# Performance work log

Measured on AMD Instinct MI355X. Metric: run time of the kernel, lower is better.

Reference implementation:

```python
import jax, jax.numpy as jnp
import numpy as np

N_NODES = 100000
N_EDGES = 1600000
F_IN, HIDDEN, N_CLASS = 256, 64, 2


def _gcn_conv(x, W, b, src, dst, norm, n):
    # PyG GCNConv: linear (no bias) -> normalized scatter-add -> bias
    h = x @ W                                  # [N, out]
    msg = h[src] * norm[:, None]               # gather + scale, [E+N, out]
    agg = jax.ops.segment_sum(msg, dst, num_segments=n)
    return agg + b


def setup_inputs() -> dict:
    key = jax.random.key(0)
    ks = jax.random.split(key, 8)
    x = jax.random.normal(ks[0], (N_NODES, F_IN), dtype=jnp.float32)
    edge_index = jax.random.randint(ks[1], (2, N_EDGES), 0, N_NODES, dtype=jnp.int32)
    W1 = jax.random.normal(ks[2], (F_IN, HIDDEN), dtype=jnp.float32) / np.sqrt(F_IN).astype(np.float32)
    b1 = jnp.zeros((HIDDEN,), dtype=jnp.float32)
    W2 = jax.random.normal(ks[3], (HIDDEN, HIDDEN), dtype=jnp.float32) / np.sqrt(HIDDEN).astype(np.float32)
    b2 = jnp.zeros((HIDDEN,), dtype=jnp.float32)
    W3 = jax.random.normal(ks[4], (HIDDEN, N_CLASS), dtype=jnp.float32) / np.sqrt(HIDDEN).astype(np.float32)
    b3 = jnp.zeros((N_CLASS,), dtype=jnp.float32)
    return {"x": x, "edge_index": edge_index, "W1": W1, "b1": b1, "W2": W2, "b2": b2, "W3": W3, "b3": b3}


def reference(x, edge_index, W1, b1, W2, b2, W3, b3):
    n = x.shape[0]
    # add self-loops (GCNConv default)
    loops = jnp.arange(n, dtype=edge_index.dtype)
    src = jnp.concatenate([edge_index[0], loops])
    dst = jnp.concatenate([edge_index[1], loops])
    # symmetric normalization D^-1/2 A_hat D^-1/2
    deg = jax.ops.segment_sum(jnp.ones_like(src, dtype=x.dtype), dst, num_segments=n)
    deg_inv_sqrt = jnp.where(deg > 0, jax.lax.rsqrt(jnp.maximum(deg, 1.0)), 0.0)
    norm = deg_inv_sqrt[src] * deg_inv_sqrt[dst]
    # layer 1 + relu (dropout is identity in eval mode)
    h = jax.nn.relu(_gcn_conv(x, W1, b1, src, dst, norm, n))
    # layer 2 + relu
    h = jax.nn.relu(_gcn_conv(h, W2, b2, src, dst, norm, n))
    # output layer + log_softmax
    h = _gcn_conv(h, W3, b3, src, dst, norm, n)
    return jax.nn.log_softmax(h, axis=1)
```

## Files before the change

kernel.cpp:

```cpp
#include <hip/hip_runtime.h>
#include <math.h>

#define F_IN 256
#define HID  64
#define BSH  8
#define BSPAN 256
#define CHUNK 4096
#define NBK_MAX 512

typedef __bf16   bf16x8 __attribute__((ext_vector_type(8)));
typedef float    floatx4 __attribute__((ext_vector_type(4)));
typedef _Float16 half8 __attribute__((ext_vector_type(8)));
typedef _Float16 half4v __attribute__((ext_vector_type(4)));

__global__ __launch_bounds__(256) void k_hist(const int* __restrict__ dst,
                                              int* __restrict__ cntT,
                                              int E, int NCH, int NBK) {
    __shared__ int hist[NBK_MAX];
    int t = threadIdx.x, c = blockIdx.x;
    hist[t] = 0; hist[t + 256] = 0;
    __syncthreads();
    int base = c * CHUNK;
#pragma unroll 4
    for (int j = 0; j < CHUNK / 256; j++) {
        int e = base + j * 256 + t;
        if (e < E) atomicAdd(&hist[dst[e] >> BSH], 1);
    }
    __syncthreads();
    for (int b = t; b < NBK; b += 256) cntT[b * NCH + c] = hist[b];
}

__global__ __launch_bounds__(256) void k_scanA(const int* __restrict__ cntT,
                                               int* __restrict__ off,
                                               int* __restrict__ partials, int S) {
    __shared__ int sh[256];
    int tid = threadIdx.x;
    int base = blockIdx.x * 1024 + tid * 4;
    int v[4];
    int s = 0;
#pragma unroll
    for (int j = 0; j < 4; j++) {
        int idx = base + j;
        v[j] = (idx < S) ? cntT[idx] : 0;
        s += v[j];
    }
    sh[tid] = s;
    __syncthreads();
    int mysum = s;
    for (int o = 1; o < 256; o <<= 1) {
        int tv = (tid >= o) ? sh[tid - o] : 0;
        __syncthreads();
        sh[tid] += tv;
        __syncthreads();
    }
    int pref = sh[tid] - mysum;
#pragma unroll
    for (int j = 0; j < 4; j++) {
        int idx = base + j;
        if (idx < S) off[idx] = pref;
        pref += v[j];
    }
    if (tid == 255) partials[blockIdx.x] = sh[255];
}

__global__ void k_scanB(int* __restrict__ partials, int* __restrict__ off,
                        int nblk, int S) {
    if (blockIdx.x == 0 && threadIdx.x == 0) {
        int run = 0;
        for (int b = 0; b < nblk; b++) { int t = partials[b]; partials[b] = run; run += t; }
        off[S] = run;
    }
}

__global__ void k_scanC(int* __restrict__ off, const int* __restrict__ partials, int S) {
    int i = blockIdx.x * blockDim.x + threadIdx.x;
    if (i < S) off[i] += partials[i >> 10];
}

__global__ __launch_bounds__(256) void k_sortwrite(const int* __restrict__ src,
                                                   const int* __restrict__ dst,
                                                   const int* __restrict__ off,
                                                   int* __restrict__ ebuf,
                                                   int E, int NCH, int NBK) {
    __shared__ int cur[NBK_MAX];
    int t = threadIdx.x, c = blockIdx.x;
    for (int b = t; b < NBK; b += 256) cur[b] = off[b * NCH + c];
    __syncthreads();
    int base = c * CHUNK;
#pragma unroll 4
    for (int j = 0; j < CHUNK / 256; j++) {
        int e = base + j * 256 + t;
        if (e < E) {
            int s = src[e];
            int d = dst[e];
            int pos = atomicAdd(&cur[d >> BSH], 1);
            ebuf[pos] = (s << BSH) | (d & (BSPAN - 1));
        }
    }
}

__global__ __launch_bounds__(256) void k_bucket_csr(const int* __restrict__ off,
                                                    const int* __restrict__ ebuf,
                                                    int* __restrict__ rp,
                                                    float* __restrict__ dinv,
                                                    int* __restrict__ esrc,
                                                    int N, int NCH, int NBK) {
    __shared__ int cnt[BSPAN];
    __shared__ int sh[BSPAN];
    int b = blockIdx.x, t = threadIdx.x;
    int base = off[b * NCH];
    int end  = off[(b + 1) * NCH];

    cnt[t] = 0;
    __syncthreads();
    for (int i = base + t; i < end; i += 256) atomicAdd(&cnt[ebuf[i] & (BSPAN - 1)], 1);
    __syncthreads();

    int c = cnt[t];
    sh[t] = c;
    __syncthreads();
    for (int o = 1; o < 256; o <<= 1) {
        int tv = (t >= o) ? sh[t - o] : 0;
        __syncthreads();
        sh[t] += tv;
        __syncthreads();
    }
    int excl = sh[t] - c;

    int node = (b << BSH) + t;
    if (node < N) {
        rp[node] = base + excl;
        dinv[node] = rsqrtf((float)(1 + c));
    }
    if (b == NBK - 1) {
        if (t == 0) rp[N] = end;
        if (t < 16) esrc[end + t] = 0;
    }
    __syncthreads();

    cnt[t] = base + excl;
    __syncthreads();
    for (int i = base + t; i < end; i += 256) {
        int v = ebuf[i];
        int p = atomicAdd(&cnt[v & (BSPAN - 1)], 1);
        esrc[p] = ((v >> BSH) << 6) | (v & 63);
    }
}

__global__ __launch_bounds__(256) void k_prepw(const float* __restrict__ W1,
                                               __bf16* __restrict__ f1h, __bf16* __restrict__ f1l,
                                               const float* __restrict__ W2,
                                               __bf16* __restrict__ f2h, __bf16* __restrict__ f2l) {
    int t = threadIdx.x + blockIdx.x * blockDim.x;
    for (int idx = t; idx < 16384; idx += 2048) {
        int j = idx & 7, lane = (idx >> 3) & 63, ch2 = (idx >> 9) & 7, c = idx >> 12;
        int k = ch2 * 32 + (lane >> 4) * 8 + j, col = c * 16 + (lane & 15);
        float w = W1[k * 64 + col];
        __bf16 h = (__bf16)w;
        f1h[idx] = h; f1l[idx] = (__bf16)(w - (float)h);
    }
    for (int idx = t; idx < 4096; idx += 2048) {
        int j = idx & 7, lane = (idx >> 3) & 63, ch2 = (idx >> 9) & 1, c = idx >> 10;
        int k = ch2 * 32 + (lane >> 4) * 8 + j, col = c * 16 + (lane & 15);
        float w = W2[k * 64 + col];
        __bf16 h = (__bf16)w;
        f2h[idx] = h; f2l[idx] = (__bf16)(w - (float)h);
    }
}

__global__ __launch_bounds__(256) void k_gemm1(const float* __restrict__ A,
                                               const __bf16* __restrict__ BfH,
                                               const __bf16* __restrict__ BfL,
                                               const float* __restrict__ dinv,
                                               _Float16* __restrict__ C, int nrows) {
    constexpr int K = 256, KC = 64, NCHK = 4, NCH32 = 8;
    __shared__ float As[2][64 * KC];

    const int t = threadIdx.x;
    const int wave = t >> 6, lane = t & 63;
    const int m = lane & 15, q = lane >> 4;
    const int row0 = blockIdx.x * 64;

    const int s_sub = lane >> 4;
    const int s_seg = lane & 15;

    auto stage = [&](int ch, int buf) {
#pragma unroll
        for (int j = 0; j < 4; j++) {
            int lr = wave * 16 + j * 4 + s_sub;
            int gr = row0 + lr; if (gr > nrows - 1) gr = nrows - 1;
            int gs = (s_seg - lr) & 15;
            const float* g = A + (size_t)gr * K + ch * KC + gs * 4;
            float* l = &As[buf][(size_t)lr * KC + s_seg * 4];
            __builtin_amdgcn_global_load_lds(
                (const __attribute__((address_space(1))) void*)g,
                (__attribute__((address_space(3))) void*)l, 16, 0, 0);
        }
    };

    floatx4 acc[4] = {{0.f, 0.f, 0.f, 0.f}, {0.f, 0.f, 0.f, 0.f},
                      {0.f, 0.f, 0.f, 0.f}, {0.f, 0.f, 0.f, 0.f}};

    stage(0, 0);
    __syncthreads();

    for (int ch = 0; ch < NCHK; ch++) {
        if (ch + 1 < NCHK) stage(ch + 1, (ch + 1) & 1);

        const float* arow = &As[ch & 1][(size_t)(wave * 16 + m) * KC];
#pragma unroll
        for (int jj = 0; jj < 2; jj++) {
            int ch2 = ch * 2 + jj;
            int s0 = jj * 8 + q * 2;
            float4 v0 = *(const float4*)(arow + (((s0 + m) & 15) * 4));
            float4 v1 = *(const float4*)(arow + (((s0 + 1 + m) & 15) * 4));
            float af[8] = {v0.x, v0.y, v0.z, v0.w, v1.x, v1.y, v1.z, v1.w};
            bf16x8 ah, al;
#pragma unroll
            for (int j = 0; j < 8; j++) {
                __bf16 h = (__bf16)af[j];
                ah[j] = h;
                al[j] = (__bf16)(af[j] - (float)h);
            }
#pragma unroll
            for (int c = 0; c < 4; c++) {
                const bf16x8 bh = *(const bf16x8*)(BfH + ((size_t)(c * NCH32 + ch2) * 64 + lane) * 8);
                const bf16x8 bl = *(const bf16x8*)(BfL + ((size_t)(c * NCH32 + ch2) * 64 + lane) * 8);
                acc[c] = __builtin_amdgcn_mfma_f32_16x16x32_bf16(ah, bh, acc[c], 0, 0, 0);
                acc[c] = __builtin_amdgcn_mfma_f32_16x16x32_bf16(al, bh, acc[c], 0, 0, 0);
                acc[c] = __builtin_amdgcn_mfma_f32_16x16x32_bf16(ah, bl, acc[c], 0, 0, 0);
            }
        }
        __syncthreads();
    }

#pragma unroll
    for (int i = 0; i < 4; i++) {
        int r = row0 + wave * 16 + q * 4 + i;
        if (r < nrows) {
            float di = dinv[r];
#pragma unroll
            for (int c = 0; c < 4; c++)
                C[(size_t)r * 64 + c * 16 + m] = (_Float16)(acc[c][i] * di);
        }
    }
}

__global__ __launch_bounds__(256) void k_gemm2(const _Float16* __restrict__ A,
                                               const __bf16* __restrict__ BfH,
                                               const __bf16* __restrict__ BfL,
                                               const float* __restrict__ dinv,
                                               _Float16* __restrict__ C, int nrows) {
    __shared__ _Float16 As[64 * 64];
    const int t = threadIdx.x;
    const int wave = t >> 6, lane = t & 63;
    const int m = lane & 15, q = lane >> 4;
    const int row0 = blockIdx.x * 64;

#pragma unroll
    for (int j = 0; j < 2; j++) {
        int lr = j * 32 + wave * 8 + (lane >> 3);
        int p  = lane & 7;
        int gr = row0 + lr; if (gr > nrows - 1) gr = nrows - 1;
        int gs = (p - lr) & 7;
        const _Float16* g = A + (size_t)gr * 64 + gs * 8;
        _Float16* l = &As[(size_t)lr * 64 + p * 8];
        __builtin_amdgcn_global_load_lds(
            (const __attribute__((address_space(1))) void*)g,
            (__attribute__((address_space(3))) void*)l, 16, 0, 0);
    }
    __syncthreads();

    floatx4 acc[4] = {{0.f, 0.f, 0.f, 0.f}, {0.f, 0.f, 0.f, 0.f},
                      {0.f, 0.f, 0.f, 0.f}, {0.f, 0.f, 0.f, 0.f}};

    const _Float16* arow = &As[(size_t)(wave * 16 + m) * 64];
#pragma unroll
    for (int jj = 0; jj < 2; jj++) {
        int s0 = jj * 4 + q;
        half8 v = *(const half8*)(arow + (((s0 + m) & 7) * 8));
        bf16x8 ah, al;
#pragma unroll
        for (int j = 0; j < 8; j++) {
            float f = (float)v[j];
            __bf16 h = (__bf16)f;
            ah[j] = h;
            al[j] = (__bf16)(f - (float)h);
        }
#pragma unroll
        for (int c = 0; c < 4; c++) {
            const bf16x8 bh = *(const bf16x8*)(BfH + ((size_t)(c * 2 + jj) * 64 + lane) * 8);
            const bf16x8 bl = *(const bf16x8*)(BfL + ((size_t)(c * 2 + jj) * 64 + lane) * 8);
            acc[c] = __builtin_amdgcn_mfma_f32_16x16x32_bf16(ah, bh, acc[c], 0, 0, 0);
            acc[c] = __builtin_amdgcn_mfma_f32_16x16x32_bf16(al, bh, acc[c], 0, 0, 0);
            acc[c] = __builtin_amdgcn_mfma_f32_16x16x32_bf16(ah, bl, acc[c], 0, 0, 0);
        }
    }

#pragma unroll
    for (int i = 0; i < 4; i++) {
        int r = row0 + wave * 16 + q * 4 + i;
        if (r < nrows) {
            float di = dinv[r];
#pragma unroll
            for (int c = 0; c < 4; c++)
                C[(size_t)r * 64 + c * 16 + m] = (_Float16)(acc[c][i] * di);
        }
    }
}

template <int MODE>
__global__ __launch_bounds__(256) void k_aggE(const _Float16* __restrict__ hs,
                                              const float* __restrict__ dinv,
                                              const int* __restrict__ rp,
                                              const int* __restrict__ esrc,
                                              const float* __restrict__ bias,
                                              const float* __restrict__ W3,
                                              void* __restrict__ out, int n) {
    constexpr int NPB = 64;
    constexpr int LDW = 68;
    __shared__ float acc[NPB * LDW];

    const int t = threadIdx.x;
    const int wv = t >> 6, lane = t & 63;
    const int qe = lane >> 4, fg = lane & 15;
    const int nb = blockIdx.x * NPB;
    const int ne = min(nb + NPB, n);

    for (int i = t; i < NPB * LDW; i += 256) acc[i] = 0.f;

    const int eb0 = rp[nb];
    const int eb1 = rp[ne];
    __syncthreads();

    const int L  = eb1 - eb0;
    const int wl = (L + 3) >> 2;
    const int wa = eb0 + wv * wl;
    const int wb = min(wa + wl, eb1);
    const int ql = (wl + 3) >> 2;
    const int qa = wa + qe * ql;
    const int qb = min(qa + ql, wb);

    int cur = -1;
    floatx4 r = {0.f, 0.f, 0.f, 0.f};
    for (int e = qa; e < qb; e += 8) {
        int ev[8]; half4v v[8];
#pragma unroll
        for (int u = 0; u < 8; u++) {
            ev[u] = esrc[e + u];
            v[u]  = *(const half4v*)(hs + (size_t)(ev[u] >> 6) * 64 + fg * 4);
        }
#pragma unroll
        for (int u = 0; u < 8; u++) {
            if (e + u < qb) {
                int row = ev[u] & 63;
                float f0 = (float)v[u][0], f1 = (float)v[u][1];
                float f2 = (float)v[u][2], f3 = (float)v[u][3];
                if (row != cur) {
                    if (cur >= 0) {
                        float* a = &acc[cur * LDW + fg * 4];
                        atomicAdd(a + 0, r[0]); atomicAdd(a + 1, r[1]);
                        atomicAdd(a + 2, r[2]); atomicAdd(a + 3, r[3]);
                    }
                    cur = row;
                    r[0] = f0; r[1] = f1; r[2] = f2; r[3] = f3;
                } else {
                    r[0] += f0; r[1] += f1; r[2] += f2; r[3] += f3;
                }
            }
        }
    }
    if (cur >= 0) {
        float* a = &acc[cur * LDW + fg * 4];
        atomicAdd(a + 0, r[0]); atomicAdd(a + 1, r[1]);
        atomicAdd(a + 2, r[2]); atomicAdd(a + 3, r[3]);
    }
    __syncthreads();

    if (MODE == 0) {
#pragma unroll
        for (int it = 0; it < 4; it++) {
            int nl = it * 16 + (t >> 4);
            int node = nb + nl;
            if (node < n) {
                int f = (t & 15) * 4;
                float dii = dinv[node];
                floatx4 av = *(const floatx4*)&acc[nl * LDW + f];
                half4v sv = *(const half4v*)(hs + (size_t)node * 64 + f);
                float4 b4 = ((const float4*)bias)[t & 15];
                float v0 = fmaxf((av[0] + (float)sv[0]) * dii + b4.x, 0.f);
                float v1 = fmaxf((av[1] + (float)sv[1]) * dii + b4.y, 0.f);
                float v2 = fmaxf((av[2] + (float)sv[2]) * dii + b4.z, 0.f);
                float v3 = fmaxf((av[3] + (float)sv[3]) * dii + b4.w, 0.f);
                half4v o4;
                o4[0] = (_Float16)v0; o4[1] = (_Float16)v1;
                o4[2] = (_Float16)v2; o4[3] = (_Float16)v3;
                *(half4v*)((_Float16*)out + (size_t)node * 64 + f) = o4;
            }
        }
    } else {
        for (int it = 0; it < 16; it++) {
            int nl = it * 4 + wv;
            int node = nb + nl;
            if (node >= n) break;
            float dii = dinv[node];
            float a = acc[nl * LDW + lane] + (float)hs[(size_t)node * 64 + lane];
            a = fmaxf(a * dii + bias[lane], 0.f);
            float2 w = ((const float2*)W3)[lane];
            float p0 = a * w.x, p1 = a * w.y;
#pragma unroll
            for (int o = 1; o <= 32; o <<= 1) {
                p0 += __shfl_xor(p0, o, 64);
                p1 += __shfl_xor(p1, o, 64);
            }
            if (lane == 0) ((float2*)out)[node] = make_float2(p0 * dii, p1 * dii);
        }
    }
}

__global__ __launch_bounds__(256) void k_final(const float2* __restrict__ h3s,
                                               const float* __restrict__ dinv,
                                               const int* __restrict__ rp,
                                               const int* __restrict__ esrc,
                                               const float* __restrict__ b3,
                                               float* __restrict__ out, int n) {
    int i = blockIdx.x * blockDim.x + threadIdx.x;
    if (i >= n) return;
    float dii = dinv[i];
    float2 h = h3s[i];
    float ax = h.x, ay = h.y;
    float bx = 0.f, by = 0.f, cx = 0.f, cy = 0.f, dx = 0.f, dy = 0.f;
    int e0 = rp[i], e1 = rp[i + 1];
    for (int e = e0; e < e1; e += 4) {
        int last = e1 - 1;
        int s0 = esrc[e] >> 6;
        int s1 = esrc[min(e + 1, last)] >> 6;
        int s2 = esrc[min(e + 2, last)] >> 6;
        int s3 = esrc[min(e + 3, last)] >> 6;
        float2 v0 = h3s[s0];
        float2 v1 = h3s[s1];
        float2 v2 = h3s[s2];
        float2 v3 = h3s[s3];
        ax += v0.x; ay += v0.y;
        bx += (e + 1 <= last) ? v1.x : 0.f; by += (e + 1 <= last) ? v1.y : 0.f;
        cx += (e + 2 <= last) ? v2.x : 0.f; cy += (e + 2 <= last) ? v2.y : 0.f;
        dx += (e + 3 <= last) ? v3.x : 0.f; dy += (e + 3 <= last) ? v3.y : 0.f;
    }
    float l0 = ((ax + bx) + (cx + dx)) * dii + b3[0];
    float l1 = ((ay + by) + (cy + dy)) * dii + b3[1];
    float mx = fmaxf(l0, l1);
    float lse = mx + log1pf(__expf(-fabsf(l0 - l1)));
    ((float2*)out)[i] = make_float2(l0 - lse, l1 - lse);
}

extern "C" void kernel_launch(void* const* d_in, const int* in_sizes, int n_in,
                              void* d_out, int out_size, void* d_ws, size_t ws_size,
                              hipStream_t stream) {
    const float* x   = (const float*)d_in[0];
    const int*   ei  = (const int*)d_in[1];
    const float* W1  = (const float*)d_in[2];
    const float* b1  = (const float*)d_in[3];
    const float* W2  = (const float*)d_in[4];
    const float* b2  = (const float*)d_in[5];
    const float* W3  = (const float*)d_in[6];
    const float* b3  = (const float*)d_in[7];
    float* out = (float*)d_out;

    const int N = in_sizes[0] / F_IN;
    const int E = in_sizes[1] / 2;
    const int* src = ei;
    const int* dst = ei + E;

    const int NBK = (N + BSPAN - 1) / BSPAN;
    const int NCH = (E + CHUNK - 1) / CHUNK;
    const int S   = NBK * NCH;

    char* p = (char*)d_ws;
    auto alloc = [&](size_t bytes) -> void* {
        void* r = (void*)p;
        p += (bytes + 255) & ~(size_t)255;
        return r;
    };
    int*      cntT     = (int*)alloc((size_t)S * 4);
    int*      off      = (int*)alloc((size_t)(S + 1) * 4);
    int*      partials = (int*)alloc(4096);
    int*      ebuf     = (int*)alloc((size_t)E * 4);
    int*      esrc     = (int*)alloc((size_t)(E + 64) * 4);
    int*      rp       = (int*)alloc((size_t)(N + 1) * 4);
    float*    dinv     = (float*)alloc((size_t)N * 4);
    _Float16* bufA     = (_Float16*)alloc((size_t)N * HID * 2);
    _Float16* bufB     = (_Float16*)alloc((size_t)N * HID * 2);
    float*    h3       = (float*)alloc((size_t)N * 2 * 4);
    __bf16*   f1h      = (__bf16*)alloc(16384 * 2);
    __bf16*   f1l      = (__bf16*)alloc(16384 * 2);
    __bf16*   f2h      = (__bf16*)alloc(4096 * 2);
    __bf16*   f2l      = (__bf16*)alloc(4096 * 2);

    const int T = 256;
    int scanBlocks = (S + 1023) / 1024;

    k_prepw<<<8, T, 0, stream>>>(W1, f1h, f1l, W2, f2h, f2l);

    k_hist<<<NCH, T, 0, stream>>>(dst, cntT, E, NCH, NBK);
    k_scanA<<<scanBlocks, T, 0, stream>>>(cntT, off, partials, S);
    k_scanB<<<1, 64, 0, stream>>>(partials, off, scanBlocks, S);
    k_scanC<<<(S + T - 1) / T, T, 0, stream>>>(off, partials, S);
    k_sortwrite<<<NCH, T, 0, stream>>>(src, dst, off, ebuf, E, NCH, NBK);
    k_bucket_csr<<<NBK, T, 0, stream>>>(off, ebuf, rp, dinv, esrc, N, NCH, NBK);

    int gemmBlocks = (N + 63) / 64;
    int aggBlocks  = (N + 63) / 64;
    k_gemm1<<<gemmBlocks, T, 0, stream>>>(x, f1h, f1l, dinv, bufA, N);
    k_aggE<0><<<aggBlocks, T, 0, stream>>>(bufA, dinv, rp, esrc, b1, nullptr, bufB, N);

    k_gemm2<<<gemmBlocks, T, 0, stream>>>(bufB, f2h, f2l, dinv, bufA, N);
    k_aggE<1><<<aggBlocks, T, 0, stream>>>(bufA, dinv, rp, esrc, b2, W3, h3, N);

    k_final<<<(N + T - 1) / T, T, 0, stream>>>((const float2*)h3, dinv, rp, esrc, b3, out, N);
}
```

Before: 406.6 us.

## Restructure edge aggregation: 32-node blocks, 8-wide half loads, double-buffered gathers

The aggregation kernel now handles 32 nodes per block instead of 64. Each lane covers 8 features with half8 loads, and the block's edge range is split into 32 segments, one per group of 8 lanes. Gathers are double-buffered in groups of four, so the next loads are in flight while the current group is accumulated. The packed edge encoding now stores the local row in 5 bits instead of 6 to match the smaller block, with matching shifts in the CSR build and final kernel. The aim is wider memory transactions and more memory-level parallelism, at the cost of more blocks and more flushes into shared-memory atomics.

```diff
diff --git a/kernel.cpp b/kernel.cpp
--- a/kernel.cpp
+++ b/kernel.cpp
@@ -143,7 +143,7 @@
     for (int i = base + t; i < end; i += 256) {
         int v = ebuf[i];
         int p = atomicAdd(&cnt[v & (BSPAN - 1)], 1);
-        esrc[p] = ((v >> BSH) << 6) | (v & 63);
+        esrc[p] = ((v >> BSH) << 5) | (v & 31);
     }
 }
 
@@ -309,6 +309,25 @@
     }
 }
 
+#define LOADB(EVa, EVb, EVc, EVd, Va, Vb, Vc, Vd, E) do {                     \
+    int _x0 = min((E),     sbm1);                                             \
+    int _x1 = min((E) + 1, sbm1);                                             \
+    int _x2 = min((E) + 2, sbm1);                                             \
+    int _x3 = min((E) + 3, sbm1);                                             \
+    EVa = esrc[_x0]; EVb = esrc[_x1]; EVc = esrc[_x2]; EVd = esrc[_x3];       \
+    Va = *(const half8*)(hs + (size_t)(EVa >> 5) * 64 + f8 * 8);              \
+    Vb = *(const half8*)(hs + (size_t)(EVb >> 5) * 64 + f8 * 8);              \
+    Vc = *(const half8*)(hs + (size_t)(EVc >> 5) * 64 + f8 * 8);              \
+    Vd = *(const half8*)(hs + (size_t)(EVd >> 5) * 64 + f8 * 8);              \
+} while (0)
+
+#define ACCB(EVa, EVb, EVc, EVd, Va, Vb, Vc, Vd, E) do {                      \
+    if ((E)     < sb) step(EVa, Va);                                          \
+    if ((E) + 1 < sb) step(EVb, Vb);                                          \
+    if ((E) + 2 < sb) step(EVc, Vc);                                          \
+    if ((E) + 3 < sb) step(EVd, Vd);                                          \
+} while (0)
+
 template <int MODE>
 __global__ __launch_bounds__(256) void k_aggE(const _Float16* __restrict__ hs,
                                               const float* __restrict__ dinv,
@@ -317,13 +336,14 @@
                                               const float* __restrict__ bias,
                                               const float* __restrict__ W3,
                                               void* __restrict__ out, int n) {
-    constexpr int NPB = 64;
+    constexpr int NPB = 32;
     constexpr int LDW = 68;
     __shared__ float acc[NPB * LDW];
 
     const int t = threadIdx.x;
     const int wv = t >> 6, lane = t & 63;
-    const int qe = lane >> 4, fg = lane & 15;
+    const int qe = lane >> 3;
+    const int f8 = lane & 7;
     const int nb = blockIdx.x * NPB;
     const int ne = min(nb + NPB, n);
 
@@ -333,87 +353,95 @@
     const int eb1 = rp[ne];
     __syncthreads();
 
-    const int L  = eb1 - eb0;
-    const int wl = (L + 3) >> 2;
-    const int wa = eb0 + wv * wl;
-    const int wb = min(wa + wl, eb1);
-    const int ql = (wl + 3) >> 2;
-    const int qa = wa + qe * ql;
-    const int qb = min(qa + ql, wb);
+    const int L   = eb1 - eb0;
+    const int sl  = (L + 31) >> 5;
+    const int sid = wv * 8 + qe;
+    const int sa  = eb0 + sid * sl;
+    const int sb  = min(sa + sl, eb1);
 
     int cur = -1;
-    floatx4 r = {0.f, 0.f, 0.f, 0.f};
-    for (int e = qa; e < qb; e += 8) {
-        int ev[8]; half4v v[8];
-#pragma unroll
-        for (int u = 0; u < 8; u++) {
-            ev[u] = esrc[e + u];
-            v[u]  = *(const half4v*)(hs + (size_t)(ev[u] >> 6) * 64 + fg * 4);
-        }
-#pragma unroll
-        for (int u = 0; u < 8; u++) {
-            if (e + u < qb) {
-                int row = ev[u] & 63;
-                float f0 = (float)v[u][0], f1 = (float)v[u][1];
-                float f2 = (float)v[u][2], f3 = (float)v[u][3];
-                if (row != cur) {
-                    if (cur >= 0) {
-                        float* a = &acc[cur * LDW + fg * 4];
-                        atomicAdd(a + 0, r[0]); atomicAdd(a + 1, r[1]);
-                        atomicAdd(a + 2, r[2]); atomicAdd(a + 3, r[3]);
-                    }
-                    cur = row;
-                    r[0] = f0; r[1] = f1; r[2] = f2; r[3] = f3;
-                } else {
-                    r[0] += f0; r[1] += f1; r[2] += f2; r[3] += f3;
-                }
+    float a0 = 0.f, a1 = 0.f, a2 = 0.f, a3 = 0.f;
+    float a4 = 0.f, a5 = 0.f, a6 = 0.f, a7 = 0.f;
+
+    auto flush = [&]() {
+        float* ap = &acc[cur * LDW + f8 * 8];
+        atomicAdd(ap + 0, a0); atomicAdd(ap + 1, a1);
+        atomicAdd(ap + 2, a2); atomicAdd(ap + 3, a3);
+        atomicAdd(ap + 4, a4); atomicAdd(ap + 5, a5);
+        atomicAdd(ap + 6, a6); atomicAdd(ap + 7, a7);
+    };
+    auto step = [&](int ev, half8 v) {
+        int row = ev & 31;
+        float f0 = (float)v[0], f1 = (float)v[1], f2 = (float)v[2], f3 = (float)v[3];
+        float f4 = (float)v[4], f5 = (float)v[5], f6 = (float)v[6], f7 = (float)v[7];
+        if (row != cur) {
+            if (cur >= 0) flush();
+            cur = row;
+            a0 = f0; a1 = f1; a2 = f2; a3 = f3;
+            a4 = f4; a5 = f5; a6 = f6; a7 = f7;
+        } else {
+            a0 += f0; a1 += f1; a2 += f2; a3 += f3;
+            a4 += f4; a5 += f5; a6 += f6; a7 += f7;
+        }
+    };
+
+    if (sa < sb) {
+        const int sbm1 = sb - 1;
+        int eA0, eA1, eA2, eA3; half8 vA0, vA1, vA2, vA3;
+        int eB0, eB1, eB2, eB3; half8 vB0, vB1, vB2, vB3;
+        int e = sa;
+        LOADB(eA0, eA1, eA2, eA3, vA0, vA1, vA2, vA3, e);
+        for (; e + 8 < sb; e += 8) {
+            LOADB(eB0, eB1, eB2, eB3, vB0, vB1, vB2, vB3, e + 4);
+            ACCB(eA0, eA1, eA2, eA3, vA0, vA1, vA2, vA3, e);
+            LOADB(eA0, eA1, eA2, eA3, vA0, vA1, vA2, vA3, e + 8);
+            ACCB(eB0, eB1, eB2, eB3, vB0, vB1, vB2, vB3, e + 4);
+        }
+        ACCB(eA0, eA1, eA2, eA3, vA0, vA1, vA2, vA3, e);
+        if (e + 4 < sb) {
+            LOADB(eB0, eB1, eB2, eB3, vB0, vB1, vB2, vB3, e + 4);
+            ACCB(eB0, eB1, eB2, eB3, vB0, vB1, vB2, vB3, e + 4);
+        }
+        if (cur >= 0) flush();
+    }
+    __syncthreads();
+
+    if (MODE == 0) {
+        int nl = t >> 3, f = (t & 7) * 8;
+        int node = nb + nl;
+        if (node < n) {
+            float dii = dinv[node];
+            const float* ap = &acc[nl * LDW + f];
+            half8 sv = *(const half8*)(hs + (size_t)node * 64 + f);
+            float4 b0 = ((const float4*)bias)[(t & 7) * 2];
+            float4 b1 = ((const float4*)bias)[(t & 7) * 2 + 1];
+            float bb[8] = {b0.x, b0.y, b0.z, b0.w, b1.x, b1.y, b1.z, b1.w};
+            half8 o;
+#pragma unroll
+            for (int j = 0; j < 8; j++) {
+                float val = (ap[j] + (float)sv[j]) * dii + bb[j];
+                o[j] = (_Float16)fmaxf(val, 0.f);
             }
-        }
-    }
-    if (cur >= 0) {
-        float* a = &acc[cur * LDW + fg * 4];
-        atomicAdd(a + 0, r[0]); atomicAdd(a + 1, r[1]);
-        atomicAdd(a + 2, r[2]); atomicAdd(a + 3, r[3]);
-    }
-    __syncthreads();
-
-    if (MODE == 0) {
-#pragma unroll
-        for (int it = 0; it < 4; it++) {
-            int nl = it * 16 + (t >> 4);
+            *(half8*)((_Float16*)out + (size_t)node * 64 + f) = o;
+        }
+    } else {
+#pragma unroll
+        for (int it = 0; it < 8; it++) {
+            int nl = it * 4 + wv;
             int node = nb + nl;
             if (node < n) {
-                int f = (t & 15) * 4;
                 float dii = dinv[node];
-                floatx4 av = *(const floatx4*)&acc[nl * LDW + f];
-                half4v sv = *(const half4v*)(hs + (size_t)node * 64 + f);
-                float4 b4 = ((const float4*)bias)[t & 15];
-                float v0 = fmaxf((av[0] + (float)sv[0]) * dii + b4.x, 0.f);
-                float v1 = fmaxf((av[1] + (float)sv[1]) * dii + b4.y, 0.f);
-                float v2 = fmaxf((av[2] + (float)sv[2]) * dii + b4.z, 0.f);
-                float v3 = fmaxf((av[3] + (float)sv[3]) * dii + b4.w, 0.f);
-                half4v o4;
-                o4[0] = (_Float16)v0; o4[1] = (_Float16)v1;
-                o4[2] = (_Float16)v2; o4[3] = (_Float16)v3;
-                *(half4v*)((_Float16*)out + (size_t)node * 64 + f) = o4;
+                float a = acc[nl * LDW + lane] + (float)hs[(size_t)node * 64 + lane];
+                a = fmaxf(a * dii + bias[lane], 0.f);
+                float2 w = ((const float2*)W3)[lane];
+                float p0 = a * w.x, p1 = a * w.y;
+#pragma unroll
+                for (int o = 1; o <= 32; o <<= 1) {
+                    p0 += __shfl_xor(p0, o, 64);
+                    p1 += __shfl_xor(p1, o, 64);
+                }
+                if (lane == 0) ((float2*)out)[node] = make_float2(p0 * dii, p1 * dii);
             }
-        }
-    } else {
-        for (int it = 0; it < 16; it++) {
-            int nl = it * 4 + wv;
-            int node = nb + nl;
-            if (node >= n) break;
-            float dii = dinv[node];
-            float a = acc[nl * LDW + lane] + (float)hs[(size_t)node * 64 + lane];
-            a = fmaxf(a * dii + bias[lane], 0.f);
-            float2 w = ((const float2*)W3)[lane];
-            float p0 = a * w.x, p1 = a * w.y;
-#pragma unroll
-            for (int o = 1; o <= 32; o <<= 1) {
-                p0 += __shfl_xor(p0, o, 64);
-                p1 += __shfl_xor(p1, o, 64);
-            }
-            if (lane == 0) ((float2*)out)[node] = make_float2(p0 * dii, p1 * dii);
         }
     }
 }
@@ -433,10 +461,10 @@
     int e0 = rp[i], e1 = rp[i + 1];
     for (int e = e0; e < e1; e += 4) {
         int last = e1 - 1;
-        int s0 = esrc[e] >> 6;
-        int s1 = esrc[min(e + 1, last)] >> 6;
-        int s2 = esrc[min(e + 2, last)] >> 6;
-        int s3 = esrc[min(e + 3, last)] >> 6;
+        int s0 = esrc[e] >> 5;
+        int s1 = esrc[min(e + 1, last)] >> 5;
+        int s2 = esrc[min(e + 2, last)] >> 5;
+        int s3 = esrc[min(e + 3, last)] >> 5;
         float2 v0 = h3s[s0];
         float2 v1 = h3s[s1];
         float2 v2 = h3s[s2];
@@ -509,7 +537,7 @@
     k_bucket_csr<<<NBK, T, 0, stream>>>(off, ebuf, rp, dinv, esrc, N, NCH, NBK);
 
     int gemmBlocks = (N + 63) / 64;
-    int aggBlocks  = (N + 63) / 64;
+    int aggBlocks  = (N + 31) / 32;
     k_gemm1<<<gemmBlocks, T, 0, stream>>>(x, f1h, f1l, dinv, bufA, N);
     k_aggE<0><<<aggBlocks, T, 0, stream>>>(bufA, dinv, rp, esrc, b1, nullptr, bufB, N);
 
```

Result: slower. 439.0 us (+8.0%).

## Store hidden features as four 16-column planes and restructure edge aggregation per plane

Applied to the files above, without the earlier changes.

The GEMM outputs and aggregation inputs move from row-major [N,64] fp16 to four planar [N,16] slices. Each plane is 32 bytes per node, so a pair of lanes covers one node per plane. The aggregation kernel now gives each lane pair a contiguous edge segment (128 segments per block) and loops over the four planes. Each lane gathers 16-byte half8 vectors, keeping the gathered working set per pass smaller and more cache-friendly. The cost is re-reading the edge indices four times, and the longer per-lane segments risk load imbalance and more LDS atomic flushes.

```diff
diff --git a/kernel.cpp b/kernel.cpp
--- a/kernel.cpp
+++ b/kernel.cpp
@@ -11,7 +11,6 @@
 typedef __bf16   bf16x8 __attribute__((ext_vector_type(8)));
 typedef float    floatx4 __attribute__((ext_vector_type(4)));
 typedef _Float16 half8 __attribute__((ext_vector_type(8)));
-typedef _Float16 half4v __attribute__((ext_vector_type(4)));
 
 __global__ __launch_bounds__(256) void k_hist(const int* __restrict__ dst,
                                               int* __restrict__ cntT,
@@ -180,6 +179,7 @@
     const int wave = t >> 6, lane = t & 63;
     const int m = lane & 15, q = lane >> 4;
     const int row0 = blockIdx.x * 64;
+    const size_t N16 = (size_t)nrows * 16;
 
     const int s_sub = lane >> 4;
     const int s_seg = lane & 15;
@@ -241,7 +241,7 @@
             float di = dinv[r];
 #pragma unroll
             for (int c = 0; c < 4; c++)
-                C[(size_t)r * 64 + c * 16 + m] = (_Float16)(acc[c][i] * di);
+                C[(size_t)c * N16 + (size_t)r * 16 + m] = (_Float16)(acc[c][i] * di);
         }
     }
 }
@@ -256,6 +256,7 @@
     const int wave = t >> 6, lane = t & 63;
     const int m = lane & 15, q = lane >> 4;
     const int row0 = blockIdx.x * 64;
+    const size_t N16 = (size_t)nrows * 16;
 
 #pragma unroll
     for (int j = 0; j < 2; j++) {
@@ -263,7 +264,7 @@
         int p  = lane & 7;
         int gr = row0 + lr; if (gr > nrows - 1) gr = nrows - 1;
         int gs = (p - lr) & 7;
-        const _Float16* g = A + (size_t)gr * 64 + gs * 8;
+        const _Float16* g = A + (size_t)(gs >> 1) * N16 + (size_t)gr * 16 + (gs & 1) * 8;
         _Float16* l = &As[(size_t)lr * 64 + p * 8];
         __builtin_amdgcn_global_load_lds(
             (const __attribute__((address_space(1))) void*)g,
@@ -304,10 +305,37 @@
             float di = dinv[r];
 #pragma unroll
             for (int c = 0; c < 4; c++)
-                C[(size_t)r * 64 + c * 16 + m] = (_Float16)(acc[c][i] * di);
-        }
-    }
-}
+                C[(size_t)c * N16 + (size_t)r * 16 + m] = (_Float16)(acc[c][i] * di);
+        }
+    }
+}
+
+#define FLUSH() do {                                                          \
+    float* ap = accph + cur * LDW;                                            \
+    atomicAdd(ap + 0, a0); atomicAdd(ap + 1, a1);                             \
+    atomicAdd(ap + 2, a2); atomicAdd(ap + 3, a3);                             \
+    atomicAdd(ap + 4, a4); atomicAdd(ap + 5, a5);                             \
+    atomicAdd(ap + 6, a6); atomicAdd(ap + 7, a7);                             \
+} while (0)
+
+#define STEPE(W, V, COND) do {                                                \
+    if (COND) {                                                               \
+        int row = (W) & 63;                                                   \
+        float f0 = (float)(V)[0], f1 = (float)(V)[1];                         \
+        float f2 = (float)(V)[2], f3 = (float)(V)[3];                         \
+        float f4 = (float)(V)[4], f5 = (float)(V)[5];                         \
+        float f6 = (float)(V)[6], f7 = (float)(V)[7];                         \
+        if (row != cur) {                                                     \
+            if (cur >= 0) FLUSH();                                            \
+            cur = row;                                                        \
+            a0 = f0; a1 = f1; a2 = f2; a3 = f3;                               \
+            a4 = f4; a5 = f5; a6 = f6; a7 = f7;                               \
+        } else {                                                              \
+            a0 += f0; a1 += f1; a2 += f2; a3 += f3;                           \
+            a4 += f4; a5 += f5; a6 += f6; a7 += f7;                           \
+        }                                                                     \
+    }                                                                         \
+} while (0)
 
 template <int MODE>
 __global__ __launch_bounds__(256) void k_aggE(const _Float16* __restrict__ hs,
@@ -323,9 +351,11 @@
 
     const int t = threadIdx.x;
     const int wv = t >> 6, lane = t & 63;
-    const int qe = lane >> 4, fg = lane & 15;
+    const int qe = lane >> 1;
+    const int f8 = lane & 1;
     const int nb = blockIdx.x * NPB;
     const int ne = min(nb + NPB, n);
+    const size_t N16 = (size_t)n * 16;
 
     for (int i = t; i < NPB * LDW; i += 256) acc[i] = 0.f;
 
@@ -333,87 +363,81 @@
     const int eb1 = rp[ne];
     __syncthreads();
 
-    const int L  = eb1 - eb0;
-    const int wl = (L + 3) >> 2;
-    const int wa = eb0 + wv * wl;
-    const int wb = min(wa + wl, eb1);
-    const int ql = (wl + 3) >> 2;
-    const int qa = wa + qe * ql;
-    const int qb = min(qa + ql, wb);
-
-    int cur = -1;
-    floatx4 r = {0.f, 0.f, 0.f, 0.f};
-    for (int e = qa; e < qb; e += 8) {
-        int ev[8]; half4v v[8];
-#pragma unroll
-        for (int u = 0; u < 8; u++) {
-            ev[u] = esrc[e + u];
-            v[u]  = *(const half4v*)(hs + (size_t)(ev[u] >> 6) * 64 + fg * 4);
-        }
-#pragma unroll
-        for (int u = 0; u < 8; u++) {
-            if (e + u < qb) {
-                int row = ev[u] & 63;
-                float f0 = (float)v[u][0], f1 = (float)v[u][1];
-                float f2 = (float)v[u][2], f3 = (float)v[u][3];
-                if (row != cur) {
-                    if (cur >= 0) {
-                        float* a = &acc[cur * LDW + fg * 4];
-                        atomicAdd(a + 0, r[0]); atomicAdd(a + 1, r[1]);
-                        atomicAdd(a + 2, r[2]); atomicAdd(a + 3, r[3]);
-                    }
-                    cur = row;
-                    r[0] = f0; r[1] = f1; r[2] = f2; r[3] = f3;
-                } else {
-                    r[0] += f0; r[1] += f1; r[2] += f2; r[3] += f3;
-                }
+    const int L   = eb1 - eb0;
+    const int sl  = (L + 127) >> 7;
+    const int sid = wv * 32 + qe;
+    const int sa  = eb0 + sid * sl;
+    const int sb  = min(sa + sl, eb1);
+
+    if (sa < sb) {
+        const int sbm1 = sb - 1;
+        for (int ph = 0; ph < 4; ph++) {
+            const _Float16* __restrict__ plane = hs + (size_t)ph * N16 + f8 * 8;
+            float* __restrict__ accph = acc + ph * 16 + f8 * 8;
+            int cur = -1;
+            float a0 = 0.f, a1 = 0.f, a2 = 0.f, a3 = 0.f;
+            float a4 = 0.f, a5 = 0.f, a6 = 0.f, a7 = 0.f;
+            for (int e = sa; e < sb; e += 4) {
+                int x1 = min(e + 1, sbm1);
+                int x2 = min(e + 2, sbm1);
+                int x3 = min(e + 3, sbm1);
+                int w0 = esrc[e], w1 = esrc[x1], w2 = esrc[x2], w3 = esrc[x3];
+                half8 v0 = *(const half8*)(plane + (size_t)(unsigned)(w0 >> 6) * 16);
+                half8 v1 = *(const half8*)(plane + (size_t)(unsigned)(w1 >> 6) * 16);
+                half8 v2 = *(const half8*)(plane + (size_t)(unsigned)(w2 >> 6) * 16);
+                half8 v3 = *(const half8*)(plane + (size_t)(unsigned)(w3 >> 6) * 16);
+                STEPE(w0, v0, true);
+                STEPE(w1, v1, e + 1 < sb);
+                STEPE(w2, v2, e + 2 < sb);
+                STEPE(w3, v3, e + 3 < sb);
             }
-        }
-    }
-    if (cur >= 0) {
-        float* a = &acc[cur * LDW + fg * 4];
-        atomicAdd(a + 0, r[0]); atomicAdd(a + 1, r[1]);
-        atomicAdd(a + 2, r[2]); atomicAdd(a + 3, r[3]);
+            FLUSH();
+        }
     }
     __syncthreads();
 
     if (MODE == 0) {
-#pragma unroll
-        for (int it = 0; it < 4; it++) {
-            int nl = it * 16 + (t >> 4);
-            int node = nb + nl;
-            if (node < n) {
-                int f = (t & 15) * 4;
-                float dii = dinv[node];
-                floatx4 av = *(const floatx4*)&acc[nl * LDW + f];
-                half4v sv = *(const half4v*)(hs + (size_t)node * 64 + f);
-                float4 b4 = ((const float4*)bias)[t & 15];
-                float v0 = fmaxf((av[0] + (float)sv[0]) * dii + b4.x, 0.f);
-                float v1 = fmaxf((av[1] + (float)sv[1]) * dii + b4.y, 0.f);
-                float v2 = fmaxf((av[2] + (float)sv[2]) * dii + b4.z, 0.f);
-                float v3 = fmaxf((av[3] + (float)sv[3]) * dii + b4.w, 0.f);
-                half4v o4;
-                o4[0] = (_Float16)v0; o4[1] = (_Float16)v1;
-                o4[2] = (_Float16)v2; o4[3] = (_Float16)v3;
-                *(half4v*)((_Float16*)out + (size_t)node * 64 + f) = o4;
+        int nl = t >> 2, ph = t & 3;
+        int node = nb + nl;
+        if (node < n) {
+            float dii = dinv[node];
+            const float* ap = &acc[nl * LDW + ph * 16];
+            const _Float16* sp = hs + (size_t)ph * N16 + (size_t)node * 16;
+            _Float16* op = (_Float16*)out + (size_t)ph * N16 + (size_t)node * 16;
+            const float4* bp = (const float4*)(bias + ph * 16);
+            float4 b0 = bp[0], b1 = bp[1], b2 = bp[2], b3 = bp[3];
+            float bb[16] = {b0.x, b0.y, b0.z, b0.w, b1.x, b1.y, b1.z, b1.w,
+                            b2.x, b2.y, b2.z, b2.w, b3.x, b3.y, b3.z, b3.w};
+            half8 s0 = *(const half8*)sp;
+            half8 s1 = *(const half8*)(sp + 8);
+            half8 o0, o1;
+#pragma unroll
+            for (int j = 0; j < 8; j++) {
+                o0[j] = (_Float16)fmaxf((ap[j] + (float)s0[j]) * dii + bb[j], 0.f);
+                o1[j] = (_Float16)fmaxf((ap[8 + j] + (float)s1[j]) * dii + bb[8 + j], 0.f);
             }
+            *(half8*)op = o0;
+            *(half8*)(op + 8) = o1;
         }
     } else {
+#pragma unroll
         for (int it = 0; it < 16; it++) {
             int nl = it * 4 + wv;
             int node = nb + nl;
-            if (node >= n) break;
-            float dii = dinv[node];
-            float a = acc[nl * LDW + lane] + (float)hs[(size_t)node * 64 + lane];
-            a = fmaxf(a * dii + bias[lane], 0.f);
-            float2 w = ((const float2*)W3)[lane];
-            float p0 = a * w.x, p1 = a * w.y;
-#pragma unroll
-            for (int o = 1; o <= 32; o <<= 1) {
-                p0 += __shfl_xor(p0, o, 64);
-                p1 += __shfl_xor(p1, o, 64);
+            if (node < n) {
+                float dii = dinv[node];
+                float self = (float)hs[(size_t)(lane >> 4) * N16 + (size_t)node * 16 + (lane & 15)];
+                float a = acc[nl * LDW + lane] + self;
+                a = fmaxf(a * dii + bias[lane], 0.f);
+                float2 w = ((const float2*)W3)[lane];
+                float p0 = a * w.x, p1 = a * w.y;
+#pragma unroll
+                for (int o = 1; o <= 32; o <<= 1) {
+                    p0 += __shfl_xor(p0, o, 64);
+                    p1 += __shfl_xor(p1, o, 64);
+                }
+                if (lane == 0) ((float2*)out)[node] = make_float2(p0 * dii, p1 * dii);
             }
-            if (lane == 0) ((float2*)out)[node] = make_float2(p0 * dii, p1 * dii);
         }
     }
 }
```

Result: slower. 519.8 us (+27.8%).
